# Kernel tuning notes

Measured on AMD Instinct MI355X. Metric: run time of the kernel, lower is better.

Reference implementation:

```python
import jax, jax.numpy as jnp
import numpy as np

B, T, D = 4, 256, 768
NG_PER = 4          # gaussians per embedding token
OUT_DIM = 3         # color channels
EPS = 1e-6
CHUNK = 64          # gaussians processed per scan step (avoids B*N*H*W tensor)


def setup_inputs() -> dict:
    key = jax.random.key(0)
    k1, k2, k3 = jax.random.split(key, 3)
    feature = jax.random.normal(k1, (B, T, D), jnp.float32)
    # proj weight init: normal(0, 0.01)
    proj_w = jax.random.normal(k2, (NG_PER * (6 + OUT_DIM), D), jnp.float32) * 0.01
    # bias init: randn*0.01, positions slots = 0, log_scale slots = -4
    bias = jax.random.normal(k3, (NG_PER, 6 + OUT_DIM), jnp.float32) * 0.01
    bias = bias.at[:, :2].set(0.0).at[:, 2:4].set(-4.0)
    proj_b = bias.reshape(-1)
    return {"feature": feature, "proj_w": proj_w, "proj_b": proj_b, "H": 256, "W": 256}


def _splat(positions, i00, i01, i11, alphas, colors, xg, yg):
    # positions [B,N,2], i** [B,N], alphas [B,N], colors [B,N,C], xg/yg [H,W]
    Bn, N = alphas.shape
    nck = N // CHUNK

    def resh(a):  # [B,N,...] -> [nck, B, CHUNK, ...]
        return jnp.moveaxis(a.reshape(Bn, nck, CHUNK, *a.shape[2:]), 1, 0)

    xs = tuple(map(resh, (positions, i00, i01, i11, alphas, colors)))
    Hh, Ww = xg.shape
    res0 = jnp.zeros((Bn, colors.shape[-1], Hh, Ww), positions.dtype)
    ws0 = jnp.zeros((Bn, Hh, Ww), positions.dtype)

    def body(carry, chunk):
        res, ws = carry
        pos, a00, a01, a11, al, col = chunk
        dx = xg[None, None] - pos[..., 0][:, :, None, None]   # [B,CHUNK,H,W]
        dy = yg[None, None] - pos[..., 1][:, :, None, None]
        q = (a00[:, :, None, None] * dx * dx
             + 2.0 * a01[:, :, None, None] * dx * dy
             + a11[:, :, None, None] * dy * dy)
        w = jnp.exp(-0.5 * q) * al[:, :, None, None]
        res = res + jnp.einsum('bnhw,bnc->bchw', w, col)
        ws = ws + w.sum(axis=1)
        return (res, ws), None

    (res, ws), _ = jax.lax.scan(body, (res0, ws0), xs)
    return res / (ws + EPS)[:, None, :, :]


def reference(feature, proj_w, proj_b, H, W):
    # projection to per-gaussian params: [B,T,n*(6+C)] -> [B, T*n, 6+C]
    gs = feature @ proj_w.T + proj_b
    gs = gs.reshape(B, T * NG_PER, 6 + OUT_DIM)
    positions = gs[..., :2]
    log_scales = gs[..., 2:4]
    rot = gs[..., 4]
    alphas = jax.nn.sigmoid(gs[..., 5])
    colors = gs[..., 6:]
    scales = jnp.exp(log_scales)

    # covariance = R S S^T R^T + eps*I, inverted analytically (2x2)
    cos, sin = jnp.cos(rot), jnp.sin(rot)
    sx2 = scales[..., 0] ** 2
    sy2 = scales[..., 1] ** 2
    c00 = cos * cos * sx2 + sin * sin * sy2 + EPS
    c01 = cos * sin * (sx2 - sy2)
    c11 = sin * sin * sx2 + cos * cos * sy2 + EPS
    det = c00 * c11 - c01 * c01
    i00 = c11 / det
    i01 = -c01 / det
    i11 = c00 / det

    # xy grid honoring aspect ratio (xy_grid staticmethod)
    ar = H / W
    hr = ar ** 0.5
    wr = 1.0 / hr
    xg = jnp.broadcast_to(jnp.linspace(-wr, wr, W, dtype=jnp.float32)[None, :], (H, W))
    yg = jnp.broadcast_to(jnp.linspace(-hr, hr, H, dtype=jnp.float32)[:, None], (H, W))

    return _splat(positions, i00, i01, i11, alphas, colors, xg, yg)
```

## Files before the change

kernel.cpp:

```cpp
#include <hip/hip_runtime.h>
#include <math.h>

#define HH 256
#define WW 256
#define NB 4
#define NG 1024
#define DD 768
#define TH_CULL 36.0f
#define TPB 256
#define CH 256

#if __has_builtin(__builtin_amdgcn_exp2f)
#define EXP2(x) __builtin_amdgcn_exp2f(x)
#else
#define EXP2(x) exp2f(x)
#endif


__global__ __launch_bounds__(256) void param_kernel(
    const float* __restrict__ feature, const float* __restrict__ proj_w,
    const float* __restrict__ proj_b, float* __restrict__ params)
{
    __shared__ float frow[DD];
    __shared__ float gsv[36];
    const int bt  = blockIdx.x;
    const int tid = threadIdx.x;

    if (tid < DD / 4) {
        ((float4*)frow)[tid] = ((const float4*)(feature + bt * DD))[tid];
    }
    __syncthreads();

    const int wave = tid >> 6, lane = tid & 63;
    for (int i = 0; i < 9; ++i) {
        const int k = wave * 9 + i;
        const float* wrow = proj_w + k * DD;
        float s = 0.f;
        #pragma unroll
        for (int j = 0; j < DD / 64; ++j)
            s = fmaf(frow[lane + j * 64], wrow[lane + j * 64], s);
        #pragma unroll
        for (int off = 32; off; off >>= 1) s += __shfl_xor(s, off, 64);
        if (lane == 0) gsv[k] = s + proj_b[k];
    }
    __syncthreads();

    if (tid < 4) {
        const float* g = gsv + tid * 9;
        const float px = g[0], py = g[1];
        const float sx = expf(g[2]), sy = expf(g[3]);
        const float sx2 = sx * sx, sy2 = sy * sy;
        const float cs = cosf(g[4]), sn = sinf(g[4]);
        const float c00 = cs * cs * sx2 + sn * sn * sy2 + 1e-6f;
        const float c01 = cs * sn * (sx2 - sy2);
        const float c11 = sn * sn * sx2 + cs * cs * sy2 + 1e-6f;
        const float det = c00 * c11 - c01 * c01;
        const float i00 = c11 / det, i01 = -c01 / det, i11 = c00 / det;
        const float F = 0.72134752044448170368f;
        const float e00 = -F * i00;
        const float e01 = -2.f * F * i01;
        const float e11 = -F * i11;
        const float la = -log2f(1.f + expf(-g[5]));
        float* o = params + (bt * 4 + tid) * 12;
        o[0] = px;  o[1] = py;  o[2] = e00; o[3] = e01;
        o[4] = e11; o[5] = la;  o[6] = g[6]; o[7] = g[7];
        o[8] = g[8];
        o[9] = sqrtf(-(e00 + e11));
        o[10] = 0.f; o[11] = 0.f;
    }
}

__global__ __launch_bounds__(TPB) void splat_kernel(
    const float* __restrict__ params, float* __restrict__ out)
{
    __shared__ int   slist[NG];
    __shared__ float sp[CH * 12 + 48];
    __shared__ float red[48][64];
    __shared__ int   scount;

    const int blk  = blockIdx.x;
    const int tlin = blk >> 2;
    const int b    = blk & 3;
    const int tl   = (int)(__brev((unsigned)tlin) >> 24);
    const int ty   = tl >> 4, tx = tl & 15;
    const int tid  = threadIdx.x;
    const int lane = tid & 63;
    const int w4   = tid >> 6;

    if (tid == 0) scount = 0;
    __syncthreads();

    const float s2 = 2.f / 255.f;
    const float cx = -1.f + s2 * ((float)(tx * 16) + 7.5f);
    const float cy = -1.f + s2 * ((float)(ty * 16) + 7.5f);
    const float rt = s2 * 7.5f * 1.41421356f;

    const float* gp = params + b * NG * 12;

    for (int k = 0; k < 4; ++k) {
        const int gi = k * 256 + tid;
        const float4 p0 = *(const float4*)(gp + gi * 12);
        const float4 p1 = *(const float4*)(gp + gi * 12 + 4);
        const float rsq = gp[gi * 12 + 9];
        const float dx = cx - p0.x, dy = cy - p0.y;
        const float qd = -(p0.z * dx * dx + p0.w * dx * dy + p1.x * dy * dy);
        const float m  = sqrtf(fmaxf(qd, 0.f));
        const float u  = m - rt * rsq;
        const bool keep = (u <= 0.f) || (u * u <= TH_CULL + p1.y);
        const unsigned long long mask = __ballot(keep);
        int base = 0;
        if (lane == 0 && mask) base = atomicAdd(&scount, (int)__popcll(mask));
        base = __shfl(base, 0, 64);
        if (keep) {
            const int off = (int)__popcll(mask & ((1ull << lane) - 1ull));
            slist[base + off] = gi;
        }
    }
    __syncthreads();
    const int cnt = scount;

    const int xl = lane & 7, yl = lane >> 3;
    const int X0 = tx * 16 + xl, Y0 = ty * 16 + yl;
    const float xg0 = -1.f + s2 * (float)X0;
    const float xg1 = -1.f + s2 * (float)(X0 + 8);
    const float yg0 = -1.f + s2 * (float)Y0;
    const float yg1 = -1.f + s2 * (float)(Y0 + 8);

    float a00=0.f,a01=0.f,a02=0.f,a03=0.f;
    float a10=0.f,a11=0.f,a12=0.f,a13=0.f;
    float a20=0.f,a21=0.f,a22=0.f,a23=0.f;
    float a30=0.f,a31=0.f,a32=0.f,a33=0.f;

    for (int cb = 0; cb < cnt; cb += CH) {
        const int n = min(CH, cnt - cb);
        __syncthreads();
        for (int i = tid; i < n * 3; i += TPB) {
            const int gl = i / 3;
            const int wd = i - gl * 3;
            const int gi = slist[cb + gl];
            *(float4*)(sp + gl * 12 + wd * 4) =
                *(const float4*)(gp + gi * 12 + wd * 4);
        }
        __syncthreads();

        int j = w4;
        float4 P0, P1; float c2v;
        if (j < n) {
            P0  = *(const float4*)(sp + j * 12);
            P1  = *(const float4*)(sp + j * 12 + 4);
            c2v = sp[j * 12 + 8];
        }
        while (j < n) {
            const int jn = j + 4;
            const float4 Q0 = *(const float4*)(sp + jn * 12);
            const float4 Q1 = *(const float4*)(sp + jn * 12 + 4);
            const float  cq = sp[jn * 12 + 8];

            const float dx0 = xg0 - P0.x, dx1 = xg1 - P0.x;
            const float ax0 = P0.z * dx0, ax1 = P0.z * dx1;
            const float dy0 = yg0 - P0.y, dy1 = yg1 - P0.y;
            const float kd0 = P0.w * dy0, kd1 = P0.w * dy1;
            const float t20 = fmaf(P1.x * dy0, dy0, P1.y);
            const float t21 = fmaf(P1.x * dy1, dy1, P1.y);

            #define PXACC(R0,R1,R2,WS,DX,AX,KD,T2) { \
                const float qq = fmaf(DX, (AX) + (KD), T2); \
                const float w = EXP2(qq); \
                WS += w; \
                R0 = fmaf(w, P1.z, R0); \
                R1 = fmaf(w, P1.w, R1); \
                R2 = fmaf(w, c2v, R2); }
            PXACC(a00,a01,a02,a03, dx0,ax0,kd0,t20)
            PXACC(a10,a11,a12,a13, dx1,ax1,kd0,t20)
            PXACC(a20,a21,a22,a23, dx0,ax0,kd1,t21)
            PXACC(a30,a31,a32,a33, dx1,ax1,kd1,t21)
            #undef PXACC

            P0 = Q0; P1 = Q1; c2v = cq;
            j = jn;
        }
    }

    __syncthreads();
    if (w4 > 0) {
        const int rb = (w4 - 1) * 16;
        red[rb +  0][lane] = a00; red[rb +  1][lane] = a01;
        red[rb +  2][lane] = a02; red[rb +  3][lane] = a03;
        red[rb +  4][lane] = a10; red[rb +  5][lane] = a11;
        red[rb +  6][lane] = a12; red[rb +  7][lane] = a13;
        red[rb +  8][lane] = a20; red[rb +  9][lane] = a21;
        red[rb + 10][lane] = a22; red[rb + 11][lane] = a23;
        red[rb + 12][lane] = a30; red[rb + 13][lane] = a31;
        red[rb + 14][lane] = a32; red[rb + 15][lane] = a33;
    }
    __syncthreads();
    if (w4 == 0) {
        #pragma unroll
        for (int s = 0; s < 3; ++s) {
            const int rb = s * 16;
            a00 += red[rb +  0][lane]; a01 += red[rb +  1][lane];
            a02 += red[rb +  2][lane]; a03 += red[rb +  3][lane];
            a10 += red[rb +  4][lane]; a11 += red[rb +  5][lane];
            a12 += red[rb +  6][lane]; a13 += red[rb +  7][lane];
            a20 += red[rb +  8][lane]; a21 += red[rb +  9][lane];
            a22 += red[rb + 10][lane]; a23 += red[rb + 11][lane];
            a30 += red[rb + 12][lane]; a31 += red[rb + 13][lane];
            a32 += red[rb + 14][lane]; a33 += red[rb + 15][lane];
        }
        const float i0 = 1.f / (a03 + 1e-6f);
        const float i1 = 1.f / (a13 + 1e-6f);
        const float i2 = 1.f / (a23 + 1e-6f);
        const float i3 = 1.f / (a33 + 1e-6f);

        const int PL = HH * WW;
        float* ob = out + (b * 3) * PL + Y0 * WW + X0;
        ob[0]                    = a00 * i0;
        ob[PL]                   = a01 * i0;
        ob[2 * PL]               = a02 * i0;
        ob[8]                    = a10 * i1;
        ob[PL + 8]               = a11 * i1;
        ob[2 * PL + 8]           = a12 * i1;
        ob[8 * WW]               = a20 * i2;
        ob[PL + 8 * WW]          = a21 * i2;
        ob[2 * PL + 8 * WW]      = a22 * i2;
        ob[8 * WW + 8]           = a30 * i3;
        ob[PL + 8 * WW + 8]      = a31 * i3;
        ob[2 * PL + 8 * WW + 8]  = a32 * i3;
    }
}

extern "C" void kernel_launch(void* const* d_in, const int* in_sizes, int n_in,
                              void* d_out, int out_size, void* d_ws, size_t ws_size,
                              hipStream_t stream) {
    const float* feature = (const float*)d_in[0];
    const float* proj_w  = (const float*)d_in[1];
    const float* proj_b  = (const float*)d_in[2];
    float* params = (float*)d_ws;
    float* out    = (float*)d_out;

    param_kernel<<<NB * 256, 256, 0, stream>>>(feature, proj_w, proj_b, params);
    splat_kernel<<<NB * 256, TPB, 0, stream>>>(params, out);
}
```

Measured before the change: 92.93 us.

## Use 512-thread persistent splat blocks and precompute squared cull limit

```diff
diff --git a/kernel.cpp b/kernel.cpp
--- a/kernel.cpp
+++ b/kernel.cpp
@@ -7,7 +7,9 @@
 #define NG 1024
 #define DD 768
 #define TH_CULL 36.0f
-#define TPB 256
+#define TPB 512
+#define NBLK 512
+#define IPB 2
 #define CH 256
 
 #if __has_builtin(__builtin_amdgcn_exp2f)
@@ -61,12 +63,14 @@
         const float e01 = -2.f * F * i01;
         const float e11 = -F * i11;
         const float la = -log2f(1.f + expf(-g[5]));
+        const float rsq = sqrtf(-(e00 + e11));
+        const float rt  = 0.08318903f;
+        const float ta  = fmaxf(TH_CULL + la, 0.f);
+        const float lim = rt * rsq + sqrtf(ta);
         float* o = params + (bt * 4 + tid) * 12;
-        o[0] = px;  o[1] = py;  o[2] = e00; o[3] = e01;
-        o[4] = e11; o[5] = la;  o[6] = g[6]; o[7] = g[7];
-        o[8] = g[8];
-        o[9] = sqrtf(-(e00 + e11));
-        o[10] = 0.f; o[11] = 0.f;
+        o[0] = px;  o[1] = py;  o[2] = e00;       o[3] = e01;
+        o[4] = e11; o[5] = lim * lim; o[6] = g[6]; o[7] = g[7];
+        o[8] = g[8]; o[9] = la; o[10] = 0.f; o[11] = 0.f;
     }
 }
 
@@ -74,158 +78,157 @@
     const float* __restrict__ params, float* __restrict__ out)
 {
     __shared__ int   slist[NG];
-    __shared__ float sp[CH * 12 + 48];
-    __shared__ float red[48][64];
+    __shared__ float sp[CH * 12 + 96];
+    __shared__ float red[112][64];
     __shared__ int   scount;
 
     const int blk  = blockIdx.x;
-    const int tlin = blk >> 2;
-    const int b    = blk & 3;
-    const int tl   = (int)(__brev((unsigned)tlin) >> 24);
-    const int ty   = tl >> 4, tx = tl & 15;
     const int tid  = threadIdx.x;
     const int lane = tid & 63;
-    const int w4   = tid >> 6;
-
-    if (tid == 0) scount = 0;
-    __syncthreads();
-
+    const int w8   = tid >> 6;
+    const int xl   = lane & 7, yl = lane >> 3;
     const float s2 = 2.f / 255.f;
-    const float cx = -1.f + s2 * ((float)(tx * 16) + 7.5f);
-    const float cy = -1.f + s2 * ((float)(ty * 16) + 7.5f);
-    const float rt = s2 * 7.5f * 1.41421356f;
-
-    const float* gp = params + b * NG * 12;
-
-    for (int k = 0; k < 4; ++k) {
-        const int gi = k * 256 + tid;
-        const float4 p0 = *(const float4*)(gp + gi * 12);
-        const float4 p1 = *(const float4*)(gp + gi * 12 + 4);
-        const float rsq = gp[gi * 12 + 9];
-        const float dx = cx - p0.x, dy = cy - p0.y;
-        const float qd = -(p0.z * dx * dx + p0.w * dx * dy + p1.x * dy * dy);
-        const float m  = sqrtf(fmaxf(qd, 0.f));
-        const float u  = m - rt * rsq;
-        const bool keep = (u <= 0.f) || (u * u <= TH_CULL + p1.y);
-        const unsigned long long mask = __ballot(keep);
-        int base = 0;
-        if (lane == 0 && mask) base = atomicAdd(&scount, (int)__popcll(mask));
-        base = __shfl(base, 0, 64);
-        if (keep) {
-            const int off = (int)__popcll(mask & ((1ull << lane) - 1ull));
-            slist[base + off] = gi;
-        }
-    }
-    __syncthreads();
-    const int cnt = scount;
-
-    const int xl = lane & 7, yl = lane >> 3;
-    const int X0 = tx * 16 + xl, Y0 = ty * 16 + yl;
-    const float xg0 = -1.f + s2 * (float)X0;
-    const float xg1 = -1.f + s2 * (float)(X0 + 8);
-    const float yg0 = -1.f + s2 * (float)Y0;
-    const float yg1 = -1.f + s2 * (float)(Y0 + 8);
-
-    float a00=0.f,a01=0.f,a02=0.f,a03=0.f;
-    float a10=0.f,a11=0.f,a12=0.f,a13=0.f;
-    float a20=0.f,a21=0.f,a22=0.f,a23=0.f;
-    float a30=0.f,a31=0.f,a32=0.f,a33=0.f;
-
-    for (int cb = 0; cb < cnt; cb += CH) {
-        const int n = min(CH, cnt - cb);
-        __syncthreads();
-        for (int i = tid; i < n * 3; i += TPB) {
-            const int gl = i / 3;
-            const int wd = i - gl * 3;
-            const int gi = slist[cb + gl];
-            *(float4*)(sp + gl * 12 + wd * 4) =
-                *(const float4*)(gp + gi * 12 + wd * 4);
-        }
-        __syncthreads();
-
-        int j = w4;
-        float4 P0, P1; float c2v;
-        if (j < n) {
-            P0  = *(const float4*)(sp + j * 12);
-            P1  = *(const float4*)(sp + j * 12 + 4);
-            c2v = sp[j * 12 + 8];
-        }
-        while (j < n) {
-            const int jn = j + 4;
-            const float4 Q0 = *(const float4*)(sp + jn * 12);
-            const float4 Q1 = *(const float4*)(sp + jn * 12 + 4);
-            const float  cq = sp[jn * 12 + 8];
-
-            const float dx0 = xg0 - P0.x, dx1 = xg1 - P0.x;
-            const float ax0 = P0.z * dx0, ax1 = P0.z * dx1;
-            const float dy0 = yg0 - P0.y, dy1 = yg1 - P0.y;
-            const float kd0 = P0.w * dy0, kd1 = P0.w * dy1;
-            const float t20 = fmaf(P1.x * dy0, dy0, P1.y);
-            const float t21 = fmaf(P1.x * dy1, dy1, P1.y);
-
-            #define PXACC(R0,R1,R2,WS,DX,AX,KD,T2) { \
-                const float qq = fmaf(DX, (AX) + (KD), T2); \
-                const float w = EXP2(qq); \
-                WS += w; \
-                R0 = fmaf(w, P1.z, R0); \
-                R1 = fmaf(w, P1.w, R1); \
-                R2 = fmaf(w, c2v, R2); }
-            PXACC(a00,a01,a02,a03, dx0,ax0,kd0,t20)
-            PXACC(a10,a11,a12,a13, dx1,ax1,kd0,t20)
-            PXACC(a20,a21,a22,a23, dx0,ax0,kd1,t21)
-            PXACC(a30,a31,a32,a33, dx1,ax1,kd1,t21)
-            #undef PXACC
-
-            P0 = Q0; P1 = Q1; c2v = cq;
-            j = jn;
-        }
-    }
-
-    __syncthreads();
-    if (w4 > 0) {
-        const int rb = (w4 - 1) * 16;
-        red[rb +  0][lane] = a00; red[rb +  1][lane] = a01;
-        red[rb +  2][lane] = a02; red[rb +  3][lane] = a03;
-        red[rb +  4][lane] = a10; red[rb +  5][lane] = a11;
-        red[rb +  6][lane] = a12; red[rb +  7][lane] = a13;
-        red[rb +  8][lane] = a20; red[rb +  9][lane] = a21;
-        red[rb + 10][lane] = a22; red[rb + 11][lane] = a23;
-        red[rb + 12][lane] = a30; red[rb + 13][lane] = a31;
-        red[rb + 14][lane] = a32; red[rb + 15][lane] = a33;
-    }
-    __syncthreads();
-    if (w4 == 0) {
-        #pragma unroll
-        for (int s = 0; s < 3; ++s) {
-            const int rb = s * 16;
-            a00 += red[rb +  0][lane]; a01 += red[rb +  1][lane];
-            a02 += red[rb +  2][lane]; a03 += red[rb +  3][lane];
-            a10 += red[rb +  4][lane]; a11 += red[rb +  5][lane];
-            a12 += red[rb +  6][lane]; a13 += red[rb +  7][lane];
-            a20 += red[rb +  8][lane]; a21 += red[rb +  9][lane];
-            a22 += red[rb + 10][lane]; a23 += red[rb + 11][lane];
-            a30 += red[rb + 12][lane]; a31 += red[rb + 13][lane];
-            a32 += red[rb + 14][lane]; a33 += red[rb + 15][lane];
-        }
-        const float i0 = 1.f / (a03 + 1e-6f);
-        const float i1 = 1.f / (a13 + 1e-6f);
-        const float i2 = 1.f / (a23 + 1e-6f);
-        const float i3 = 1.f / (a33 + 1e-6f);
-
-        const int PL = HH * WW;
-        float* ob = out + (b * 3) * PL + Y0 * WW + X0;
-        ob[0]                    = a00 * i0;
-        ob[PL]                   = a01 * i0;
-        ob[2 * PL]               = a02 * i0;
-        ob[8]                    = a10 * i1;
-        ob[PL + 8]               = a11 * i1;
-        ob[2 * PL + 8]           = a12 * i1;
-        ob[8 * WW]               = a20 * i2;
-        ob[PL + 8 * WW]          = a21 * i2;
-        ob[2 * PL + 8 * WW]      = a22 * i2;
-        ob[8 * WW + 8]           = a30 * i3;
-        ob[PL + 8 * WW + 8]      = a31 * i3;
-        ob[2 * PL + 8 * WW + 8]  = a32 * i3;
+
+    for (int s = 0; s < IPB; ++s) {
+        const int item = s * NBLK + blk;
+        const int b    = item & 3;
+        const int tl   = ((item >> 2) * 73) & 255;
+        const int ty   = tl >> 4, tx = tl & 15;
+
+        if (tid == 0) scount = 0;
+        __syncthreads();
+
+        const float cx = -1.f + s2 * ((float)(tx * 16) + 7.5f);
+        const float cy = -1.f + s2 * ((float)(ty * 16) + 7.5f);
+        const float* gp = params + b * NG * 12;
+
+        for (int k = 0; k < 2; ++k) {
+            const int gi = k * TPB + tid;
+            const float4 p0 = *(const float4*)(gp + gi * 12);
+            const float4 p1 = *(const float4*)(gp + gi * 12 + 4);
+            const float dx = cx - p0.x, dy = cy - p0.y;
+            const float qd = -fmaf(p0.z * dx, dx, fmaf(p0.w * dx, dy, p1.x * dy * dy));
+            const bool keep = (qd <= p1.y);
+            const unsigned long long mask = __ballot(keep);
+            int base = 0;
+            if (lane == 0 && mask) base = atomicAdd(&scount, (int)__popcll(mask));
+            base = __shfl(base, 0, 64);
+            if (keep) {
+                const int off = (int)__popcll(mask & ((1ull << lane) - 1ull));
+                slist[base + off] = gi;
+            }
+        }
+        __syncthreads();
+        const int cnt = scount;
+
+        const int X0 = tx * 16 + xl, Y0 = ty * 16 + yl;
+        const float xg0 = -1.f + s2 * (float)X0;
+        const float xg1 = -1.f + s2 * (float)(X0 + 8);
+        const float yg0 = -1.f + s2 * (float)Y0;
+        const float yg1 = -1.f + s2 * (float)(Y0 + 8);
+
+        float a00=0.f,a01=0.f,a02=0.f,a03=0.f;
+        float a10=0.f,a11=0.f,a12=0.f,a13=0.f;
+        float a20=0.f,a21=0.f,a22=0.f,a23=0.f;
+        float a30=0.f,a31=0.f,a32=0.f,a33=0.f;
+
+        for (int cb = 0; cb < cnt; cb += CH) {
+            const int n = min(CH, cnt - cb);
+            __syncthreads();
+            for (int i = tid; i < n * 3; i += TPB) {
+                const int gl = i / 3;
+                const int wd = i - gl * 3;
+                const int gi = slist[cb + gl];
+                *(float4*)(sp + gl * 12 + wd * 4) =
+                    *(const float4*)(gp + gi * 12 + wd * 4);
+            }
+            __syncthreads();
+
+            int j = w8;
+            float4 P0, P1; float2 P2;
+            if (j < n) {
+                P0 = *(const float4*)(sp + j * 12);
+                P1 = *(const float4*)(sp + j * 12 + 4);
+                P2 = *(const float2*)(sp + j * 12 + 8);
+            }
+            while (j < n) {
+                const int jn = j + 8;
+                const float4 Q0 = *(const float4*)(sp + jn * 12);
+                const float4 Q1 = *(const float4*)(sp + jn * 12 + 4);
+                const float2 Q2 = *(const float2*)(sp + jn * 12 + 8);
+
+                const float dx0 = xg0 - P0.x, dx1 = xg1 - P0.x;
+                const float ax0 = P0.z * dx0, ax1 = P0.z * dx1;
+                const float dy0 = yg0 - P0.y, dy1 = yg1 - P0.y;
+                const float kd0 = P0.w * dy0, kd1 = P0.w * dy1;
+                const float t20 = fmaf(P1.x * dy0, dy0, P2.y);
+                const float t21 = fmaf(P1.x * dy1, dy1, P2.y);
+
+                #define PXACC(R0,R1,R2,WS,DX,AX,KD,T2) { \
+                    const float qq = fmaf(DX, (AX) + (KD), T2); \
+                    const float w = EXP2(qq); \
+                    WS += w; \
+                    R0 = fmaf(w, P1.z, R0); \
+                    R1 = fmaf(w, P1.w, R1); \
+                    R2 = fmaf(w, P2.x, R2); }
+                PXACC(a00,a01,a02,a03, dx0,ax0,kd0,t20)
+                PXACC(a10,a11,a12,a13, dx1,ax1,kd0,t20)
+                PXACC(a20,a21,a22,a23, dx0,ax0,kd1,t21)
+                PXACC(a30,a31,a32,a33, dx1,ax1,kd1,t21)
+                #undef PXACC
+
+                P0 = Q0; P1 = Q1; P2 = Q2;
+                j = jn;
+            }
+        }
+
+        __syncthreads();
+        if (w8 > 0) {
+            const int rb = (w8 - 1) * 16;
+            red[rb +  0][lane] = a00; red[rb +  1][lane] = a01;
+            red[rb +  2][lane] = a02; red[rb +  3][lane] = a03;
+            red[rb +  4][lane] = a10; red[rb +  5][lane] = a11;
+            red[rb +  6][lane] = a12; red[rb +  7][lane] = a13;
+            red[rb +  8][lane] = a20; red[rb +  9][lane] = a21;
+            red[rb + 10][lane] = a22; red[rb + 11][lane] = a23;
+            red[rb + 12][lane] = a30; red[rb + 13][lane] = a31;
+            red[rb + 14][lane] = a32; red[rb + 15][lane] = a33;
+        }
+        __syncthreads();
+        if (w8 == 0) {
+            #pragma unroll
+            for (int r = 0; r < 7; ++r) {
+                const int rb = r * 16;
+                a00 += red[rb +  0][lane]; a01 += red[rb +  1][lane];
+                a02 += red[rb +  2][lane]; a03 += red[rb +  3][lane];
+                a10 += red[rb +  4][lane]; a11 += red[rb +  5][lane];
+                a12 += red[rb +  6][lane]; a13 += red[rb +  7][lane];
+                a20 += red[rb +  8][lane]; a21 += red[rb +  9][lane];
+                a22 += red[rb + 10][lane]; a23 += red[rb + 11][lane];
+                a30 += red[rb + 12][lane]; a31 += red[rb + 13][lane];
+                a32 += red[rb + 14][lane]; a33 += red[rb + 15][lane];
+            }
+            const float i0 = 1.f / (a03 + 1e-6f);
+            const float i1 = 1.f / (a13 + 1e-6f);
+            const float i2 = 1.f / (a23 + 1e-6f);
+            const float i3 = 1.f / (a33 + 1e-6f);
+
+            const int PL = HH * WW;
+            float* ob = out + (b * 3) * PL + Y0 * WW + X0;
+            ob[0]                    = a00 * i0;
+            ob[PL]                   = a01 * i0;
+            ob[2 * PL]               = a02 * i0;
+            ob[8]                    = a10 * i1;
+            ob[PL + 8]               = a11 * i1;
+            ob[2 * PL + 8]           = a12 * i1;
+            ob[8 * WW]               = a20 * i2;
+            ob[PL + 8 * WW]          = a21 * i2;
+            ob[2 * PL + 8 * WW]      = a22 * i2;
+            ob[8 * WW + 8]           = a30 * i3;
+            ob[PL + 8 * WW + 8]      = a31 * i3;
+            ob[2 * PL + 8 * WW + 8]  = a32 * i3;
+        }
+        __syncthreads();
     }
 }
 
@@ -239,5 +242,5 @@
     float* out    = (float*)d_out;
 
     param_kernel<<<NB * 256, 256, 0, stream>>>(feature, proj_w, proj_b, params);
-    splat_kernel<<<NB * 256, TPB, 0, stream>>>(params, out);
+    splat_kernel<<<NBLK, TPB, 0, stream>>>(params, out);
 }
```

Result: faster. 86.93 us (-6.5%).
